# Kernel tuning notes

Hardware: AMD Instinct MI355X
Metric: run time of the kernel (lower is better)

## Reference

```python
import jax, jax.numpy as jnp
import numpy as np

HEADS = 8
DIM_HEAD = 64
QUERY_DIM = 1024
CONTEXT_DIM = 768
INNER = HEADS * DIM_HEAD  # 512


def setup_inputs() -> dict:
    key = jax.random.key(0)
    ks = jax.random.split(key, 8)
    b, n, j = 4, 2048, 2048
    x = jax.random.normal(ks[0], (b, n, QUERY_DIM), dtype=jnp.float32)
    context = jax.random.normal(ks[1], (b, j, CONTEXT_DIM), dtype=jnp.float32)
    mask = jax.random.randint(ks[2], (b, j), 0, 2).astype(jnp.bool_)
    # weights stored as (in, out) so forward is x @ W (torch Linear stores transpose)
    W_q = jax.random.normal(ks[3], (QUERY_DIM, INNER), dtype=jnp.float32) / np.sqrt(QUERY_DIM)
    W_k = jax.random.normal(ks[4], (CONTEXT_DIM, INNER), dtype=jnp.float32) / np.sqrt(CONTEXT_DIM)
    W_v = jax.random.normal(ks[5], (CONTEXT_DIM, INNER), dtype=jnp.float32) / np.sqrt(CONTEXT_DIM)
    W_o = jax.random.normal(ks[6], (INNER, QUERY_DIM), dtype=jnp.float32) / np.sqrt(INNER)
    b_o = jax.random.normal(ks[7], (QUERY_DIM,), dtype=jnp.float32) * 0.01
    return {"x": x, "context": context, "mask": mask,
            "W_q": W_q, "W_k": W_k, "W_v": W_v, "W_o": W_o, "b_o": b_o}


def reference(x, context, mask, W_q, W_k, W_v, W_o, b_o):
    b, n, _ = x.shape
    j = context.shape[1]
    scale = DIM_HEAD ** -0.5
    # projections -> [b, n, h, d]
    q = (x @ W_q).reshape(b, n, HEADS, DIM_HEAD)
    k = (context @ W_k).reshape(b, j, HEADS, DIM_HEAD)
    v = (context @ W_v).reshape(b, j, HEADS, DIM_HEAD)
    # similarity [b, h, n, j]
    sim = jnp.einsum('bihd,bjhd->bhij', q, k) * scale
    max_neg = -jnp.finfo(sim.dtype).max
    sim = jnp.where(mask[:, None, None, :], sim, max_neg)
    attn = jax.nn.softmax(sim, axis=-1)
    out = jnp.einsum('bhij,bjhd->bihd', attn, v).reshape(b, n, INNER)
    return out @ W_o + b_o  # dropout is identity (p=0 / eval)
```

## Files before the change

kernel.cpp:

```cpp
#include <hip/hip_runtime.h>
#include <hip/hip_bf16.h>

typedef __attribute__((ext_vector_type(4)))  float  f32x4;
typedef __attribute__((ext_vector_type(16))) float  f32x16;
typedef __attribute__((ext_vector_type(8)))  short  bf16x8;
typedef __attribute__((ext_vector_type(4)))  int    int32x4;
typedef __attribute__((ext_vector_type(2)))  unsigned int uint32x2;

#define DEVINL static __device__ __forceinline__
#define GAS __attribute__((address_space(1)))
#define LAS __attribute__((address_space(3)))

DEVINL ushort f2bf(float f) {
  unsigned u = __builtin_bit_cast(unsigned, f);
  unsigned r = u + 0x7fffu + ((u >> 16) & 1u);
  return (ushort)(r >> 16);
}

DEVINL unsigned cvtpk(float lo, float hi) {
  unsigned r;
  asm("v_cvt_pk_bf16_f32 %0, %1, %2" : "=v"(r) : "v"(lo), "v"(hi));
  return r;
}

DEVINL void plswap(unsigned &a, unsigned &b) {
  asm("v_permlane32_swap_b32 %0, %1" : "+v"(a), "+v"(b));
}

DEVINL float fexp2(float x) { return __builtin_amdgcn_exp2f(x); }

DEVINL float bf2f(short s) {
  return __builtin_bit_cast(float, ((unsigned)(ushort)s) << 16);
}

DEVINL f32x4 mfma16(bf16x8 a, bf16x8 b, f32x4 c) {
  return __builtin_amdgcn_mfma_f32_16x16x32_bf16(a, b, c, 0, 0, 0);
}
DEVINL f32x16 mfma32(bf16x8 a, bf16x8 b, f32x16 c) {
  return __builtin_amdgcn_mfma_f32_32x32x16_bf16(a, b, c, 0, 0, 0);
}

__global__ __launch_bounds__(256)
void prep_k(const int* __restrict__ msk, float* __restrict__ mbias,
            const float* __restrict__ Wq, const float* __restrict__ Wk,
            const float* __restrict__ Wv, const float* __restrict__ Wo,
            ushort* __restrict__ WqT, ushort* __restrict__ WkT,
            ushort* __restrict__ WvT, ushort* __restrict__ WoT)
{
  __shared__ ushort Ts[64][72];
  int id = blockIdx.x;
  if (id >= 448) {
    int tid = (id - 448) * 256 + threadIdx.x;
    if (tid < 8192) mbias[tid] = msk[tid] ? 0.f : -1e30f;
    return;
  }
  const float* src; ushort* dst; int Kd, Nd, lid;
  if (id < 128)      { src = Wq; dst = WqT; Kd = 1024; Nd = 512;  lid = id; }
  else if (id < 224) { src = Wk; dst = WkT; Kd = 768;  Nd = 512;  lid = id - 128; }
  else if (id < 320) { src = Wv; dst = WvT; Kd = 768;  Nd = 512;  lid = id - 224; }
  else               { src = Wo; dst = WoT; Kd = 512;  Nd = 1024; lid = id - 320; }
  const int sh = (Nd == 512) ? 3 : 4;
  const int kb = lid >> sh, nb = lid & ((1 << sh) - 1);
  const int k0 = kb * 64, n0 = nb * 64;
  const int t = threadIdx.x;
  const int r = t >> 2, c0 = (t & 3) * 16;

  const float* sp = src + (size_t)(k0 + r) * Nd + n0 + c0;
  f32x4 v0 = *(const f32x4*)(sp);
  f32x4 v1 = *(const f32x4*)(sp + 4);
  f32x4 v2 = *(const f32x4*)(sp + 8);
  f32x4 v3 = *(const f32x4*)(sp + 12);
  #pragma unroll
  for (int e = 0; e < 4; e++) {
    Ts[c0 + e][r]      = f2bf(v0[e]);
    Ts[c0 + 4 + e][r]  = f2bf(v1[e]);
    Ts[c0 + 8 + e][r]  = f2bf(v2[e]);
    Ts[c0 + 12 + e][r] = f2bf(v3[e]);
  }
  __syncthreads();
  const int n = t >> 2, kc = (t & 3) * 16;
  bf16x8 o0 = *(const bf16x8*)&Ts[n][kc];
  bf16x8 o1 = *(const bf16x8*)&Ts[n][kc + 8];
  ushort* dp = dst + (size_t)(n0 + n) * Kd + k0 + kc;
  *(bf16x8*)dp       = o0;
  *(bf16x8*)(dp + 8) = o1;
}

template<int PHASE>
__global__ __launch_bounds__(256)
void mm_k(const float* __restrict__ xf, const float* __restrict__ cf,
          const ushort* __restrict__ WqT, const ushort* __restrict__ WkT,
          const ushort* __restrict__ WvT,
          ushort* __restrict__ Qb, ushort* __restrict__ Kb, ushort* __restrict__ VT,
          const ushort* __restrict__ AO, const ushort* __restrict__ WoT,
          float* __restrict__ out, const float* __restrict__ bias)
{
  constexpr int AST = (PHASE == 0) ? 40 : 32;
  __shared__ ushort As[2][128 * AST];
  __shared__ ushort Bs[2][128 * 32];

  const float* Af = nullptr; const ushort* Ab = nullptr; const ushort* BT;
  ushort* Cw = nullptr;
  int Kd, mode, m0, n0;
  if (PHASE == 0) {
    int id = blockIdx.x;
    id = (id & 7) * 96 + (id >> 3);
    const int which = id >> 8, local = id & 255;
    m0 = (local >> 2) * 128; n0 = (local & 3) * 128;
    if (which == 0)      { Af = xf; BT = WqT; Cw = Qb; Kd = 1024; mode = 1; }
    else if (which == 1) { Af = cf; BT = WkT; Cw = Kb; Kd = 768;  mode = 1; }
    else                 { Af = cf; BT = WvT; Cw = VT; Kd = 768;  mode = 2; }
  } else {
    int id = blockIdx.x;
    id = (id & 7) * 64 + (id >> 3);
    m0 = (id >> 3) * 128; n0 = (id & 7) * 128;
    Ab = AO; BT = WoT; Kd = 512; mode = 0;
  }

  const int t = threadIdx.x, lane = t & 63, w = t >> 6;
  const int wr = w >> 1, wc = w & 1;
  const int g = lane >> 4, ql = lane & 15;

  const int arow = t >> 1, akc = (t & 1) * 16;
  const int srowo = 16 * w + (lane >> 2);
  const int sgg = (lane & 3) ^ ((lane >> 3) & 3);

  f32x4 acc[4][4];
  #pragma unroll
  for (int i = 0; i < 4; i++)
    #pragma unroll
    for (int j = 0; j < 4; j++) acc[i][j] = (f32x4){0.f, 0.f, 0.f, 0.f};

  auto stageB = [&](int buf, int k0) {
    #pragma unroll
    for (int i = 0; i < 2; i++) {
      const int row = i * 64 + srowo;
      const ushort* bsrc = BT + (size_t)(n0 + row) * Kd + k0 + sgg * 8;
      __builtin_amdgcn_global_load_lds((const GAS void*)bsrc,
          (LAS void*)&Bs[buf][(i * 64 + 16 * w) * 32], 16, 0, 0);
    }
  };
  auto stageA_lds = [&](int buf, int k0) {
    #pragma unroll
    for (int i = 0; i < 2; i++) {
      const int row = i * 64 + srowo;
      const ushort* asrc = Ab + (size_t)(m0 + row) * Kd + k0 + sgg * 8;
      __builtin_amdgcn_global_load_lds((const GAS void*)asrc,
          (LAS void*)&As[buf][(i * 64 + 16 * w) * 32], 16, 0, 0);
    }
  };
  auto loadA_f32 = [&](int k0, f32x4 (&d)[4]) {
    const float* ap = Af + (size_t)(m0 + arow) * Kd + k0 + akc;
    d[0] = *(const f32x4*)(ap);
    d[1] = *(const f32x4*)(ap + 4);
    d[2] = *(const f32x4*)(ap + 8);
    d[3] = *(const f32x4*)(ap + 12);
  };
  auto writeA_f32 = [&](int buf, const f32x4 (&v)[4]) {
    union { unsigned u[4]; int32x4 vv; } w1_, w2_;
    w1_.u[0] = cvtpk(v[0][0], v[0][1]); w1_.u[1] = cvtpk(v[0][2], v[0][3]);
    w1_.u[2] = cvtpk(v[1][0], v[1][1]); w1_.u[3] = cvtpk(v[1][2], v[1][3]);
    w2_.u[0] = cvtpk(v[2][0], v[2][1]); w2_.u[1] = cvtpk(v[2][2], v[2][3]);
    w2_.u[2] = cvtpk(v[3][0], v[3][1]); w2_.u[3] = cvtpk(v[3][2], v[3][3]);
    ushort* dst = &As[0][0] + (size_t)buf * 128 * 40 + arow * 40 + akc;
    *(int32x4*)dst       = w1_.vv;
    *(int32x4*)(dst + 8) = w2_.vv;
  };

  const int sel = (ql >> 1) & 3;
  const int koff = (g ^ sel) * 8;
  const int NK = Kd >> 5;

  auto mfmaBlock = [&](int cur) {
    bf16x8 af[4], bfr[4];
    #pragma unroll
    for (int i = 0; i < 4; i++) {
      if (PHASE == 0)
        af[i] = *(const bf16x8*)&As[cur][(wr * 64 + i * 16 + ql) * 40 + g * 8];
      else
        af[i] = *(const bf16x8*)&As[cur][(wr * 64 + i * 16 + ql) * 32 + koff];
      bfr[i] = *(const bf16x8*)&Bs[cur][(wc * 64 + i * 16 + ql) * 32 + koff];
    }
    #pragma unroll
    for (int i = 0; i < 4; i++)
      #pragma unroll
      for (int j = 0; j < 4; j++)
        acc[i][j] = mfma16(af[i], bfr[j], acc[i][j]);
  };

  if (PHASE == 0) {
    f32x4 pS0[4], pS1[4];
    loadA_f32(0, pS0);
    writeA_f32(0, pS0);
    stageB(0, 0);
    loadA_f32(32, pS0);
    __syncthreads();

    auto bodyP0 = [&](int tt, int cur, f32x4 (&consume)[4], f32x4 (&fill)[4]) {
      const bool nb = (tt + 1 < NK);
      const bool nl = (tt + 2 < NK);
      if (nb) stageB(cur ^ 1, (tt + 1) * 32);
      __builtin_amdgcn_sched_barrier(0);
      if (nl) loadA_f32((tt + 2) * 32, fill);
      __builtin_amdgcn_sched_barrier(0);
      mfmaBlock(cur);
      if (nb) writeA_f32(cur ^ 1, consume);
      if (nl) asm volatile("s_waitcnt vmcnt(4) lgkmcnt(0)" ::: "memory");
      else    asm volatile("s_waitcnt vmcnt(0) lgkmcnt(0)" ::: "memory");
      __builtin_amdgcn_s_barrier();
      __builtin_amdgcn_sched_barrier(0);
    };
    for (int tt = 0; tt < NK; tt += 2) {
      bodyP0(tt,     0, pS0, pS1);
      bodyP0(tt + 1, 1, pS1, pS0);
    }
  } else {
    stageA_lds(0, 0);
    stageB(0, 0);
    __syncthreads();
    for (int tt = 0; tt < NK; tt++) {
      const int cur = tt & 1;
      if (tt + 1 < NK) { stageA_lds(cur ^ 1, (tt + 1) * 32); stageB(cur ^ 1, (tt + 1) * 32); }
      mfmaBlock(cur);
      __syncthreads();
    }
  }

  #pragma unroll
  for (int i = 0; i < 4; i++) {
    #pragma unroll
    for (int j = 0; j < 4; j++) {
      int col = n0 + wc * 64 + j * 16 + ql;
      #pragma unroll
      for (int r = 0; r < 4; r++) {
        int mrow = m0 + wr * 64 + i * 16 + g * 4 + r;
        float v = acc[i][j][r];
        if (PHASE == 1) {
          out[(size_t)mrow * 1024 + col] = v + bias[col];
        } else {
          int b = mrow >> 11, nn = mrow & 2047;
          int hh = col >> 6, dd = col & 63;
          size_t base = (size_t)(b * 8 + hh) * 131072;
          if (mode == 1) Cw[base + (size_t)nn * 64 + dd]   = f2bf(v);
          else           Cw[base + (size_t)dd * 2048 + nn] = f2bf(v);
        }
      }
    }
  }
}

__global__ __launch_bounds__(512)
void attn_k(const ushort* __restrict__ Qb, const ushort* __restrict__ Kb,
            const ushort* __restrict__ VT, const float* __restrict__ mb,
            ushort* __restrict__ Opart, float2* __restrict__ Ml)
{
  constexpr int CHUNK = 512, NT = CHUNK / 64;
  __shared__ ushort Ks[2][64 * 64];
  __shared__ ushort Vs[2][64 * 64];

  const int bh = blockIdx.x, b = bh >> 3;
  const int sp = blockIdx.z;
  const int jb = sp * CHUNK;
  const int t = threadIdx.x, lane = t & 63, w = t >> 6;
  const int l31 = lane & 31, hi = lane >> 5;
  const int q0 = blockIdx.y * 256 + w * 32;

  const ushort* Qh = Qb + (size_t)bh * 131072;
  const ushort* Kh = Kb + (size_t)bh * 131072;
  const ushort* Vh = VT + (size_t)bh * 131072;
  const float* mp = mb + b * 2048 + 4 * hi;

  const int srow = lane >> 3;
  const int soff = ((lane & 7) * 16) ^ ((srow & 7) << 4);

  auto stage = [&](int buf, int j0) {
    const char* kg = (const char*)Kh + ((size_t)(j0 + 8 * w + srow)) * 128 + soff;
    __builtin_amdgcn_global_load_lds((const GAS void*)kg,
        (LAS void*)&Ks[buf][8 * w * 64], 16, 0, 0);
    const char* vg = (const char*)Vh + ((size_t)(8 * w + srow)) * 4096 + (size_t)j0 * 2 + soff;
    __builtin_amdgcn_global_load_lds((const GAS void*)vg,
        (LAS void*)&Vs[buf][8 * w * 64], 16, 0, 0);
  };

  bf16x8 qf[4];
  #pragma unroll
  for (int kk = 0; kk < 4; kk++)
    qf[kk] = *(const bf16x8*)(Qh + (size_t)(q0 + l31) * 64 + kk * 16 + 8 * hi);

  union { unsigned u[4]; bf16x8 v; } ones;
  ones.u[0] = 0x3F803F80u; ones.u[1] = 0x3F803F80u;
  ones.u[2] = 0x3F803F80u; ones.u[3] = 0x3F803F80u;

  f32x16 o0 = {}, o1 = {};
  float m = -1e30f, lsum = 0.f;
  const float sc = 0.18033688011112042f;

  stage(0, jb);
  __syncthreads();

  for (int tt = 0; tt < NT; ++tt) {
    const int cur = tt & 1;
    if (tt + 1 < NT) stage(cur ^ 1, jb + (tt + 1) * 64);

    #pragma unroll
    for (int js = 0; js < 2; ++js) {
      const int jloc = js * 32;
      const int j0 = jb + tt * 64 + jloc;

      f32x4 mb0 = *(const f32x4*)(mp + j0);
      f32x4 mb1 = *(const f32x4*)(mp + j0 + 8);
      f32x4 mb2 = *(const f32x4*)(mp + j0 + 16);
      f32x4 mb3 = *(const f32x4*)(mp + j0 + 24);

      const int krow = jloc + l31;
      const unsigned rsw = (unsigned)((l31 & 7) << 4);
      const char* kbase = (const char*)&Ks[cur][0] + krow * 128;
      bf16x8 kf0 = *(const bf16x8*)(kbase + ((0  + hi * 16) ^ rsw));
      bf16x8 kf1 = *(const bf16x8*)(kbase + ((32 + hi * 16) ^ rsw));
      bf16x8 kf2 = *(const bf16x8*)(kbase + ((64 + hi * 16) ^ rsw));
      bf16x8 kf3 = *(const bf16x8*)(kbase + ((96 + hi * 16) ^ rsw));

      __builtin_amdgcn_s_setprio(1);
      f32x16 z = {};
      f32x16 s = mfma32(kf0, qf[0], z);
      s = mfma32(kf1, qf[1], s);
      s = mfma32(kf2, qf[2], s);
      s = mfma32(kf3, qf[3], s);
      __builtin_amdgcn_s_setprio(0);

      const char* vb0 = (const char*)&Vs[cur][0] + l31 * 128;
      const char* vb1 = vb0 + 32 * 128;
      const unsigned vc0 = (unsigned)((jloc * 2 + hi * 16) ^ rsw);
      const unsigned vc1 = (unsigned)((jloc * 2 + 32 + hi * 16) ^ rsw);
      bf16x8 vf00 = *(const bf16x8*)(vb0 + vc0);
      bf16x8 vf01 = *(const bf16x8*)(vb0 + vc1);
      bf16x8 vf10 = *(const bf16x8*)(vb1 + vc0);
      bf16x8 vf11 = *(const bf16x8*)(vb1 + vc1);

      float pv[16];
      #pragma unroll
      for (int e = 0; e < 4; e++) {
        pv[e]      = fmaf(s[e],      sc, mb0[e]);
        pv[4 + e]  = fmaf(s[4 + e],  sc, mb1[e]);
        pv[8 + e]  = fmaf(s[8 + e],  sc, mb2[e]);
        pv[12 + e] = fmaf(s[12 + e], sc, mb3[e]);
      }

      float t0 = fmaxf(fmaxf(pv[0],  pv[1]),  pv[2]);
      float t1 = fmaxf(fmaxf(pv[3],  pv[4]),  pv[5]);
      float t2 = fmaxf(fmaxf(pv[6],  pv[7]),  pv[8]);
      float t3 = fmaxf(fmaxf(pv[9],  pv[10]), pv[11]);
      float t4 = fmaxf(fmaxf(pv[12], pv[13]), pv[14]);
      float pm = fmaxf(fmaxf(fmaxf(t0, t1), t2), fmaxf(fmaxf(t3, t4), pv[15]));
      pm = fmaxf(pm, __shfl_xor(pm, 32));

      if (!__all(pm <= m + 8.f)) {
        float mn = fmaxf(m, pm);
        float al = fexp2(m - mn);
        lsum *= al;
        #pragma unroll
        for (int r = 0; r < 16; r++) { o0[r] *= al; o1[r] *= al; }
        m = mn;
      }

      #pragma unroll
      for (int r = 0; r < 16; r++) pv[r] = fexp2(pv[r] - m);

      unsigned pk01 = cvtpk(pv[0],  pv[1]),  pk23 = cvtpk(pv[2],  pv[3]);
      unsigned pk45 = cvtpk(pv[4],  pv[5]),  pk67 = cvtpk(pv[6],  pv[7]);
      unsigned pk89 = cvtpk(pv[8],  pv[9]),  pkAB = cvtpk(pv[10], pv[11]);
      unsigned pkCD = cvtpk(pv[12], pv[13]), pkEF = cvtpk(pv[14], pv[15]);
      plswap(pk01, pk45);
      plswap(pk23, pk67);
      plswap(pk89, pkCD);
      plswap(pkAB, pkEF);
      union { unsigned u[4]; bf16x8 v; } pf0, pf1;
      pf0.u[0] = pk01; pf0.u[1] = pk23; pf0.u[2] = pk45; pf0.u[3] = pk67;
      pf1.u[0] = pk89; pf1.u[1] = pkAB; pf1.u[2] = pkCD; pf1.u[3] = pkEF;

      __builtin_amdgcn_s_setprio(1);
      f32x16 zs = {};
      zs = mfma32(ones.v, pf0.v, zs);
      zs = mfma32(ones.v, pf1.v, zs);
      o0 = mfma32(vf00, pf0.v, o0);
      o0 = mfma32(vf01, pf1.v, o0);
      o1 = mfma32(vf10, pf0.v, o1);
      o1 = mfma32(vf11, pf1.v, o1);
      __builtin_amdgcn_s_setprio(0);
      lsum += zs[0];
    }
    __syncthreads();
  }

  float inv = lsum > 0.f ? 1.0f / lsum : 0.f;
  const int q = q0 + l31;
  ushort* op = Opart + (size_t)sp * 4194304 + ((size_t)(bh * 2048 + q)) * 64;
  #pragma unroll
  for (int grp = 0; grp < 4; grp++) {
    int d0 = grp * 8 + 4 * hi;
    uint32x2 w0, w1;
    w0[0] = cvtpk(o0[4 * grp] * inv, o0[4 * grp + 1] * inv);
    w0[1] = cvtpk(o0[4 * grp + 2] * inv, o0[4 * grp + 3] * inv);
    w1[0] = cvtpk(o1[4 * grp] * inv, o1[4 * grp + 1] * inv);
    w1[1] = cvtpk(o1[4 * grp + 2] * inv, o1[4 * grp + 3] * inv);
    *(uint32x2*)(op + d0)      = w0;
    *(uint32x2*)(op + 32 + d0) = w1;
  }
  if (hi == 0) {
    float2 v; v.x = m; v.y = lsum;
    Ml[sp * 65536 + bh * 2048 + q] = v;
  }
}

__global__ __launch_bounds__(256)
void reduce_k(const ushort* __restrict__ Opart, const float2* __restrict__ Ml,
              ushort* __restrict__ AO)
{
  const int idx = blockIdx.x * 256 + threadIdx.x;
  const int d8 = idx & 7, q = (idx >> 3) & 2047, bh = idx >> 14;
  const int b = bh >> 3, h = bh & 7;

  float2 ml[4];
  float M = -1e30f;
  #pragma unroll
  for (int s = 0; s < 4; s++) {
    ml[s] = Ml[s * 65536 + bh * 2048 + q];
    M = fmaxf(M, ml[s].x);
  }
  float wgt[4], L = 0.f;
  #pragma unroll
  for (int s = 0; s < 4; s++) {
    wgt[s] = ml[s].y * fexp2(ml[s].x - M);
    L += wgt[s];
  }
  float invL = 1.f / L;

  float acc[8] = {0.f,0.f,0.f,0.f,0.f,0.f,0.f,0.f};
  #pragma unroll
  for (int s = 0; s < 4; s++) {
    bf16x8 v = *(const bf16x8*)(Opart + (size_t)s * 4194304 +
                                ((size_t)(bh * 2048 + q)) * 64 + d8 * 8);
    float ws = wgt[s] * invL;
    #pragma unroll
    for (int e = 0; e < 8; e++) acc[e] += ws * bf2f(v[e]);
  }

  union { unsigned u[4]; int32x4 v; } pk;
  pk.u[0] = cvtpk(acc[0], acc[1]);
  pk.u[1] = cvtpk(acc[2], acc[3]);
  pk.u[2] = cvtpk(acc[4], acc[5]);
  pk.u[3] = cvtpk(acc[6], acc[7]);
  *(int32x4*)(AO + ((size_t)(b * 2048 + q)) * 512 + h * 64 + d8 * 8) = pk.v;
}

extern "C" void kernel_launch(void* const* d_in, const int* in_sizes, int n_in,
                              void* d_out, int out_size, void* d_ws, size_t ws_size,
                              hipStream_t stream)
{
  const float* x   = (const float*)d_in[0];
  const float* ctx = (const float*)d_in[1];
  const int*   mk  = (const int*)d_in[2];
  const float* Wq  = (const float*)d_in[3];
  const float* Wk  = (const float*)d_in[4];
  const float* Wv  = (const float*)d_in[5];
  const float* Wo  = (const float*)d_in[6];
  const float* bo  = (const float*)d_in[7];
  float* out = (float*)d_out;

  ushort* Qb  = (ushort*)d_ws;
  ushort* Kb  = Qb + 4194304;
  ushort* VT  = Kb + 4194304;
  ushort* WoT = VT + 4194304;
  float*  mb  = (float*)(WoT + 524288);
  ushort* R2  = WoT + 524288 + 16384;
  ushort* WqT = R2;
  ushort* WkT = WqT + 524288;
  ushort* WvT = WkT + 393216;
  ushort* Opart = WvT + 393216;
  float2* Ml    = (float2*)(Opart + 16777216);
  ushort* AO    = Qb;

  prep_k<<<480, 256, 0, stream>>>(mk, mb, Wq, Wk, Wv, Wo, WqT, WkT, WvT, WoT);
  mm_k<0><<<768, 256, 0, stream>>>(x, ctx, WqT, WkT, WvT, Qb, Kb, VT,
                                   nullptr, nullptr, nullptr, nullptr);
  attn_k<<<dim3(32, 8, 4), 512, 0, stream>>>(Qb, Kb, VT, mb, Opart, Ml);
  reduce_k<<<2048, 256, 0, stream>>>(Opart, Ml, AO);
  mm_k<1><<<512, 256, 0, stream>>>(nullptr, nullptr, nullptr, nullptr, nullptr,
                                   nullptr, nullptr, nullptr, AO, WoT, out, bo);
}
```

Before: 141.4 us.

## Fuse split-KV partial reduction into output projection GEMM A-tile loading

Removes the separate reduce_k kernel that merged the four split-KV partial outputs into AO. The output-projection GEMM now loads the four bf16 partials and their max/sum stats directly while staging the A tile, combines them in registers and writes bf16 to LDS, much as phase 0 handles its fp32 A. This saves a launch and the AO write and reread, but every one of the 8 column-tile blocks per row tile repeats the partial loads and combine math. A-tile staging also moves from async global-to-LDS copies to register loads.

```diff
diff --git a/kernel.cpp b/kernel.cpp
--- a/kernel.cpp
+++ b/kernel.cpp
@@ -92,14 +92,14 @@
           const ushort* __restrict__ WqT, const ushort* __restrict__ WkT,
           const ushort* __restrict__ WvT,
           ushort* __restrict__ Qb, ushort* __restrict__ Kb, ushort* __restrict__ VT,
-          const ushort* __restrict__ AO, const ushort* __restrict__ WoT,
+          const ushort* __restrict__ Opart, const float2* __restrict__ Ml,
+          const ushort* __restrict__ WoT,
           float* __restrict__ out, const float* __restrict__ bias)
 {
-  constexpr int AST = (PHASE == 0) ? 40 : 32;
-  __shared__ ushort As[2][128 * AST];
+  __shared__ ushort As[2][128 * 40];
   __shared__ ushort Bs[2][128 * 32];
 
-  const float* Af = nullptr; const ushort* Ab = nullptr; const ushort* BT;
+  const float* Af = nullptr; const ushort* BT;
   ushort* Cw = nullptr;
   int Kd, mode, m0, n0;
   if (PHASE == 0) {
@@ -114,7 +114,7 @@
     int id = blockIdx.x;
     id = (id & 7) * 64 + (id >> 3);
     m0 = (id >> 3) * 128; n0 = (id & 7) * 128;
-    Ab = AO; BT = WoT; Kd = 512; mode = 0;
+    BT = WoT; Kd = 512; mode = 0;
   }
 
   const int t = threadIdx.x, lane = t & 63, w = t >> 6;
@@ -138,15 +138,6 @@
       const ushort* bsrc = BT + (size_t)(n0 + row) * Kd + k0 + sgg * 8;
       __builtin_amdgcn_global_load_lds((const GAS void*)bsrc,
           (LAS void*)&Bs[buf][(i * 64 + 16 * w) * 32], 16, 0, 0);
-    }
-  };
-  auto stageA_lds = [&](int buf, int k0) {
-    #pragma unroll
-    for (int i = 0; i < 2; i++) {
-      const int row = i * 64 + srowo;
-      const ushort* asrc = Ab + (size_t)(m0 + row) * Kd + k0 + sgg * 8;
-      __builtin_amdgcn_global_load_lds((const GAS void*)asrc,
-          (LAS void*)&As[buf][(i * 64 + 16 * w) * 32], 16, 0, 0);
     }
   };
   auto loadA_f32 = [&](int k0, f32x4 (&d)[4]) {
@@ -167,6 +158,48 @@
     *(int32x4*)(dst + 8) = w2_.vv;
   };
 
+  auto loadP1 = [&](int tt, bf16x8 (&ov)[4][2], float2 (&mlv)[4]) {
+    const int h = tt >> 1;
+    const int dbase = (tt & 1) * 32 + akc;
+    const int mrow = m0 + arow;
+    const int b = mrow >> 11, q = mrow & 2047;
+    const int bhq = (b * 8 + h) * 2048 + q;
+    #pragma unroll
+    for (int s = 0; s < 4; s++) {
+      const ushort* op = Opart + (size_t)s * 4194304 + (size_t)bhq * 64 + dbase;
+      ov[s][0] = *(const bf16x8*)(op);
+      ov[s][1] = *(const bf16x8*)(op + 8);
+      mlv[s] = Ml[s * 65536 + bhq];
+    }
+  };
+  auto writeP1 = [&](int buf, const bf16x8 (&ov)[4][2], const float2 (&mlv)[4]) {
+    float M = fmaxf(fmaxf(mlv[0].x, mlv[1].x), fmaxf(mlv[2].x, mlv[3].x));
+    float wgt[4], L = 0.f;
+    #pragma unroll
+    for (int s = 0; s < 4; s++) { wgt[s] = mlv[s].y * fexp2(mlv[s].x - M); L += wgt[s]; }
+    float invL = 1.f / L;
+    float a[16];
+    #pragma unroll
+    for (int e = 0; e < 16; e++) a[e] = 0.f;
+    #pragma unroll
+    for (int s = 0; s < 4; s++) {
+      float ws = wgt[s] * invL;
+      #pragma unroll
+      for (int e = 0; e < 8; e++) {
+        a[e]     += ws * bf2f(ov[s][0][e]);
+        a[8 + e] += ws * bf2f(ov[s][1][e]);
+      }
+    }
+    union { unsigned u[4]; int32x4 vv; } w1_, w2_;
+    w1_.u[0] = cvtpk(a[0],  a[1]);  w1_.u[1] = cvtpk(a[2],  a[3]);
+    w1_.u[2] = cvtpk(a[4],  a[5]);  w1_.u[3] = cvtpk(a[6],  a[7]);
+    w2_.u[0] = cvtpk(a[8],  a[9]);  w2_.u[1] = cvtpk(a[10], a[11]);
+    w2_.u[2] = cvtpk(a[12], a[13]); w2_.u[3] = cvtpk(a[14], a[15]);
+    ushort* dst = &As[0][0] + (size_t)buf * 128 * 40 + arow * 40 + akc;
+    *(int32x4*)dst       = w1_.vv;
+    *(int32x4*)(dst + 8) = w2_.vv;
+  };
+
   const int sel = (ql >> 1) & 3;
   const int koff = (g ^ sel) * 8;
   const int NK = Kd >> 5;
@@ -175,10 +208,7 @@
     bf16x8 af[4], bfr[4];
     #pragma unroll
     for (int i = 0; i < 4; i++) {
-      if (PHASE == 0)
-        af[i] = *(const bf16x8*)&As[cur][(wr * 64 + i * 16 + ql) * 40 + g * 8];
-      else
-        af[i] = *(const bf16x8*)&As[cur][(wr * 64 + i * 16 + ql) * 32 + koff];
+      af[i]  = *(const bf16x8*)&As[cur][(wr * 64 + i * 16 + ql) * 40 + g * 8];
       bfr[i] = *(const bf16x8*)&Bs[cur][(wc * 64 + i * 16 + ql) * 32 + koff];
     }
     #pragma unroll
@@ -215,13 +245,17 @@
       bodyP0(tt + 1, 1, pS1, pS0);
     }
   } else {
-    stageA_lds(0, 0);
+    bf16x8 ov[4][2]; float2 mlv[4];
+    loadP1(0, ov, mlv);
+    writeP1(0, ov, mlv);
     stageB(0, 0);
     __syncthreads();
     for (int tt = 0; tt < NK; tt++) {
       const int cur = tt & 1;
-      if (tt + 1 < NK) { stageA_lds(cur ^ 1, (tt + 1) * 32); stageB(cur ^ 1, (tt + 1) * 32); }
+      const bool nb = (tt + 1 < NK);
+      if (nb) { stageB(cur ^ 1, (tt + 1) * 32); loadP1(tt + 1, ov, mlv); }
       mfmaBlock(cur);
+      if (nb) writeP1(cur ^ 1, ov, mlv);
       __syncthreads();
     }
   }
@@ -412,47 +446,6 @@
   }
 }
 
-__global__ __launch_bounds__(256)
-void reduce_k(const ushort* __restrict__ Opart, const float2* __restrict__ Ml,
-              ushort* __restrict__ AO)
-{
-  const int idx = blockIdx.x * 256 + threadIdx.x;
-  const int d8 = idx & 7, q = (idx >> 3) & 2047, bh = idx >> 14;
-  const int b = bh >> 3, h = bh & 7;
-
-  float2 ml[4];
-  float M = -1e30f;
-  #pragma unroll
-  for (int s = 0; s < 4; s++) {
-    ml[s] = Ml[s * 65536 + bh * 2048 + q];
-    M = fmaxf(M, ml[s].x);
-  }
-  float wgt[4], L = 0.f;
-  #pragma unroll
-  for (int s = 0; s < 4; s++) {
-    wgt[s] = ml[s].y * fexp2(ml[s].x - M);
-    L += wgt[s];
-  }
-  float invL = 1.f / L;
-
-  float acc[8] = {0.f,0.f,0.f,0.f,0.f,0.f,0.f,0.f};
-  #pragma unroll
-  for (int s = 0; s < 4; s++) {
-    bf16x8 v = *(const bf16x8*)(Opart + (size_t)s * 4194304 +
-                                ((size_t)(bh * 2048 + q)) * 64 + d8 * 8);
-    float ws = wgt[s] * invL;
-    #pragma unroll
-    for (int e = 0; e < 8; e++) acc[e] += ws * bf2f(v[e]);
-  }
-
-  union { unsigned u[4]; int32x4 v; } pk;
-  pk.u[0] = cvtpk(acc[0], acc[1]);
-  pk.u[1] = cvtpk(acc[2], acc[3]);
-  pk.u[2] = cvtpk(acc[4], acc[5]);
-  pk.u[3] = cvtpk(acc[6], acc[7]);
-  *(int32x4*)(AO + ((size_t)(b * 2048 + q)) * 512 + h * 64 + d8 * 8) = pk.v;
-}
-
 extern "C" void kernel_launch(void* const* d_in, const int* in_sizes, int n_in,
                               void* d_out, int out_size, void* d_ws, size_t ws_size,
                               hipStream_t stream)
@@ -478,13 +471,11 @@
   ushort* WvT = WkT + 393216;
   ushort* Opart = WvT + 393216;
   float2* Ml    = (float2*)(Opart + 16777216);
-  ushort* AO    = Qb;
 
   prep_k<<<480, 256, 0, stream>>>(mk, mb, Wq, Wk, Wv, Wo, WqT, WkT, WvT, WoT);
   mm_k<0><<<768, 256, 0, stream>>>(x, ctx, WqT, WkT, WvT, Qb, Kb, VT,
-                                   nullptr, nullptr, nullptr, nullptr);
+                                   nullptr, nullptr, nullptr, nullptr, nullptr);
   attn_k<<<dim3(32, 8, 4), 512, 0, stream>>>(Qb, Kb, VT, mb, Opart, Ml);
-  reduce_k<<<2048, 256, 0, stream>>>(Opart, Ml, AO);
   mm_k<1><<<512, 256, 0, stream>>>(nullptr, nullptr, nullptr, nullptr, nullptr,
-                                   nullptr, nullptr, nullptr, AO, WoT, out, bo);
-}
+                                   nullptr, nullptr, nullptr, Opart, Ml, WoT, out, bo);
+}
```

New measurement: 155.5 us. 10.0% more time.

## Triple-buffer LDS tiles to prefetch two K-steps ahead in projection GEMMs

Applied to the files above, without the earlier changes.

Moves the B tiles of the projection GEMM, and both A and B tiles of the output projection GEMM, from double to triple LDS buffering. Global-to-LDS loads are issued two K iterations ahead, and the waits use explicit vmcnt counts instead of draining all loads, so more memory latency overlaps with MFMA work. The cost is more LDS per block, which may reduce occupancy, and the fine-grained waitcnt tuning must match the actual number of outstanding loads.

```diff
diff --git a/kernel.cpp b/kernel.cpp
--- a/kernel.cpp
+++ b/kernel.cpp
@@ -96,8 +96,9 @@
           float* __restrict__ out, const float* __restrict__ bias)
 {
   constexpr int AST = (PHASE == 0) ? 40 : 32;
-  __shared__ ushort As[2][128 * AST];
-  __shared__ ushort Bs[2][128 * 32];
+  constexpr int ANB = (PHASE == 0) ? 2 : 3;
+  __shared__ ushort As[ANB][128 * AST];
+  __shared__ ushort Bs[3][128 * 32];
 
   const float* Af = nullptr; const ushort* Ab = nullptr; const ushort* BT;
   ushort* Cw = nullptr;
@@ -171,15 +172,15 @@
   const int koff = (g ^ sel) * 8;
   const int NK = Kd >> 5;
 
-  auto mfmaBlock = [&](int cur) {
+  auto mfmaBlock = [&](int ac, int bc) {
     bf16x8 af[4], bfr[4];
     #pragma unroll
     for (int i = 0; i < 4; i++) {
       if (PHASE == 0)
-        af[i] = *(const bf16x8*)&As[cur][(wr * 64 + i * 16 + ql) * 40 + g * 8];
+        af[i] = *(const bf16x8*)&As[ac][(wr * 64 + i * 16 + ql) * 40 + g * 8];
       else
-        af[i] = *(const bf16x8*)&As[cur][(wr * 64 + i * 16 + ql) * 32 + koff];
-      bfr[i] = *(const bf16x8*)&Bs[cur][(wc * 64 + i * 16 + ql) * 32 + koff];
+        af[i] = *(const bf16x8*)&As[ac][(wr * 64 + i * 16 + ql) * 32 + koff];
+      bfr[i] = *(const bf16x8*)&Bs[bc][(wc * 64 + i * 16 + ql) * 32 + koff];
     }
     #pragma unroll
     for (int i = 0; i < 4; i++)
@@ -194,35 +195,50 @@
     writeA_f32(0, pS0);
     stageB(0, 0);
     loadA_f32(32, pS0);
-    __syncthreads();
-
-    auto bodyP0 = [&](int tt, int cur, f32x4 (&consume)[4], f32x4 (&fill)[4]) {
-      const bool nb = (tt + 1 < NK);
-      const bool nl = (tt + 2 < NK);
-      if (nb) stageB(cur ^ 1, (tt + 1) * 32);
+    stageB(1, 32);
+    asm volatile("s_waitcnt vmcnt(6) lgkmcnt(0)" ::: "memory");
+    __builtin_amdgcn_s_barrier();
+
+    auto bodyP0 = [&](int tt, int acur, int bcur, int bnx,
+                      f32x4 (&consume)[4], f32x4 (&fill)[4]) {
+      const bool nb  = (tt + 1 < NK);
+      const bool nb2 = (tt + 2 < NK);
+      if (nb2) loadA_f32((tt + 2) * 32, fill);
       __builtin_amdgcn_sched_barrier(0);
-      if (nl) loadA_f32((tt + 2) * 32, fill);
+      if (nb2) stageB(bnx, (tt + 2) * 32);
       __builtin_amdgcn_sched_barrier(0);
-      mfmaBlock(cur);
-      if (nb) writeA_f32(cur ^ 1, consume);
-      if (nl) asm volatile("s_waitcnt vmcnt(4) lgkmcnt(0)" ::: "memory");
-      else    asm volatile("s_waitcnt vmcnt(0) lgkmcnt(0)" ::: "memory");
+      mfmaBlock(acur, bcur);
+      if (nb) writeA_f32(acur ^ 1, consume);
+      if (nb2) asm volatile("s_waitcnt vmcnt(6) lgkmcnt(0)" ::: "memory");
+      else     asm volatile("s_waitcnt vmcnt(0) lgkmcnt(0)" ::: "memory");
       __builtin_amdgcn_s_barrier();
       __builtin_amdgcn_sched_barrier(0);
     };
+    int bb = 0;
     for (int tt = 0; tt < NK; tt += 2) {
-      bodyP0(tt,     0, pS0, pS1);
-      bodyP0(tt + 1, 1, pS1, pS0);
+      const int b1i = (bb + 1 >= 3) ? bb - 2 : bb + 1;
+      const int b2i = (bb + 2 >= 3) ? bb - 1 : bb + 2;
+      bodyP0(tt,     0, bb,  b2i, pS0, pS1);
+      bodyP0(tt + 1, 1, b1i, bb,  pS1, pS0);
+      bb = b2i;
     }
   } else {
-    stageA_lds(0, 0);
-    stageB(0, 0);
-    __syncthreads();
+    stageA_lds(0, 0);  stageB(0, 0);
+    stageA_lds(1, 32); stageB(1, 32);
+    asm volatile("s_waitcnt vmcnt(4) lgkmcnt(0)" ::: "memory");
+    __builtin_amdgcn_s_barrier();
+    int bc = 0;
     for (int tt = 0; tt < NK; tt++) {
-      const int cur = tt & 1;
-      if (tt + 1 < NK) { stageA_lds(cur ^ 1, (tt + 1) * 32); stageB(cur ^ 1, (tt + 1) * 32); }
-      mfmaBlock(cur);
-      __syncthreads();
+      const bool nb2 = (tt + 2 < NK);
+      const int bnx = (bc + 2 >= 3) ? bc - 1 : bc + 2;
+      if (nb2) { stageA_lds(bnx, (tt + 2) * 32); stageB(bnx, (tt + 2) * 32); }
+      __builtin_amdgcn_sched_barrier(0);
+      mfmaBlock(bc, bc);
+      if (nb2) asm volatile("s_waitcnt vmcnt(4) lgkmcnt(0)" ::: "memory");
+      else     asm volatile("s_waitcnt vmcnt(0) lgkmcnt(0)" ::: "memory");
+      __builtin_amdgcn_s_barrier();
+      __builtin_amdgcn_sched_barrier(0);
+      bc = (bc + 1 >= 3) ? 0 : bc + 1;
     }
   }
 
```

New measurement: 142.6 us (median of 3 runs). About the same (+0.8%).
